# Kernel optimization log

Hardware: AMD Instinct MI355X
Metric: run time of the kernel (lower is better)

## Reference

```python
import jax, jax.numpy as jnp
import numpy as np

B, H, W, NC = 8, 64, 64, 128
INTER = NC // 2
BN_EPS = 1e-4


def setup_inputs() -> dict:
    key = jax.random.key(0)
    ks = jax.random.split(key, 6)
    s_in = 1.0 / np.sqrt(NC)
    s_w = 1.0 / np.sqrt(INTER)
    return {
        "x": jax.random.normal(ks[0], (B, H, W, NC), jnp.float32),
        "theta_w": jax.random.normal(ks[1], (NC, INTER), jnp.float32) * s_in,
        "theta_b": jnp.zeros((INTER,), jnp.float32),
        "phi_w": jax.random.normal(ks[2], (NC, INTER), jnp.float32) * s_in,
        "phi_b": jnp.zeros((INTER,), jnp.float32),
        "g_w": jax.random.normal(ks[3], (NC, INTER), jnp.float32) * s_in,
        "g_b": jnp.zeros((INTER,), jnp.float32),
        "W_w": jax.random.normal(ks[4], (INTER, NC), jnp.float32) * s_w,
        "W_b": jnp.zeros((NC,), jnp.float32),
        "bn_gamma": jnp.ones((NC,), jnp.float32),
        "bn_beta": jnp.zeros((NC,), jnp.float32),
        "bn_mean": jnp.zeros((NC,), jnp.float32),
        "bn_var": jax.random.uniform(ks[5], (NC,), jnp.float32, 0.5, 1.5),
    }


def reference(x, theta_w, theta_b, phi_w, phi_b, g_w, g_b, W_w, W_b,
              bn_gamma, bn_beta, bn_mean, bn_var):
    b, h, w, c = x.shape
    n = h * w
    # 1x1 conv projections == per-pixel GEMMs; flatten spatial to tokens
    xt = x.reshape(b, n, c)                                  # [B, N, C]
    theta = xt @ theta_w + theta_b                           # [B, N, C']
    phi = xt @ phi_w + phi_b                                 # [B, N, C']
    g = xt @ g_w + g_b                                       # [B, N, C']
    # single-head, unscaled non-local attention
    f = jnp.einsum("bnc,bmc->bnm", theta, phi)               # [B, N, N]
    attn = jax.nn.softmax(f, axis=-1)
    y = jnp.einsum("bnm,bmc->bnc", attn, g)                  # [B, N, C']
    # W: 1x1 conv back to nc + BatchNorm (inference), then residual
    wy = y @ W_w + W_b                                       # [B, N, C]
    inv = bn_gamma * jax.lax.rsqrt(bn_var + BN_EPS)
    wy = (wy - bn_mean) * inv + bn_beta
    z = wy.reshape(b, h, w, c) + x
    return z
```

## Files before the change

### kernel.cpp

```cpp
#include <hip/hip_runtime.h>
#include <math.h>

typedef _Float16 v8h __attribute__((ext_vector_type(8)));
typedef __fp16 h2 __attribute__((ext_vector_type(2)));
typedef float v4f __attribute__((ext_vector_type(4)));
typedef float v16f __attribute__((ext_vector_type(16)));

#define MFMA32(a, b, c) __builtin_amdgcn_mfma_f32_32x32x16_f16((a), (b), (c), 0, 0, 0)
#define MFMA16(a, b, c) __builtin_amdgcn_mfma_f32_16x16x32_f16((a), (b), (c), 0, 0, 0)
#define ZV4 ((v4f){0.f, 0.f, 0.f, 0.f})
#define LOG2E 1.44269504f

#define TA64(row, colb)  ((((row) * 128) + (colb)) ^ (((row) & 7) << 4))
#define TA128(row, colb) ((((row) * 256) + (colb)) ^ (((row) & 15) << 4))

#define RAW_BARRIER() do {                                        \
    asm volatile("s_waitcnt lgkmcnt(0)" ::: "memory");            \
    asm volatile("s_barrier" ::: "memory");                       \
} while (0)

__device__ __forceinline__ unsigned int pk_f16(float a, float b) {
    return __builtin_bit_cast(unsigned int, __builtin_amdgcn_cvt_pkrtz(a, b));
}
__device__ __forceinline__ void pl32swap(unsigned int& a, unsigned int& b) {
    asm("v_permlane32_swap_b32 %0, %1" : "+v"(a), "+v"(b));
}
__device__ __forceinline__ float fexp2(float x) {
    float r;
    asm("v_exp_f32 %0, %1" : "=v"(r) : "v"(x));
    return r;
}

__global__ __launch_bounds__(256) void k_prep(
    const float* __restrict__ tw, const float* __restrict__ pw,
    const float* __restrict__ gw,
    const float* __restrict__ Ww, const float* __restrict__ Wb,
    const float* __restrict__ gamma, const float* __restrict__ beta,
    const float* __restrict__ mean, const float* __restrict__ var,
    _Float16* __restrict__ Wt, _Float16* __restrict__ wallT,
    float* __restrict__ sc, float* __restrict__ bi)
{
    int gid = blockIdx.x * 256 + threadIdx.x;
    #pragma unroll
    for (int r = 0; r < 2; ++r) {
        int idx = r * 4096 + gid;
        int d = idx >> 7, c = idx & 127;
        Wt[c * 64 + d] = (_Float16)Ww[idx];
    }
    #pragma unroll
    for (int r = 0; r < 6; ++r) {
        int idx = r * 4096 + gid;
        int p = idx >> 13, rem = idx & 8191;
        int o = rem >> 7, k = rem & 127;
        const float* wm = (p == 0) ? tw : (p == 1) ? pw : gw;
        wallT[idx] = (_Float16)wm[k * 64 + o];
    }
    if (blockIdx.x == 0 && threadIdx.x < 128) {
        int c = threadIdx.x;
        float inv = gamma[c] * rsqrtf(var[c] + 1e-4f);
        sc[c] = inv;
        bi[c] = (Wb[c] - mean[c]) * inv + beta[c];
    }
}

__global__ __launch_bounds__(512, 4) void k_proj(
    const float* __restrict__ x, const _Float16* __restrict__ wallT,
    const float* __restrict__ tb, const float* __restrict__ pb,
    const float* __restrict__ gb,
    _Float16* __restrict__ theta, _Float16* __restrict__ phi,
    _Float16* __restrict__ gT)
{
    __shared__ __align__(16) _Float16 tsc[8][16 * 72];
    __shared__ __align__(16) _Float16 gblk[64][136];
    const int t = threadIdx.x;
    const int w = t >> 6, l = t & 63, h = l >> 4, lo = l & 15;
    const int tok0 = blockIdx.x * 128 + w * 16;
    _Float16* tw_l = &tsc[w][0];

    v8h xA[4];
    #pragma unroll
    for (int kc = 0; kc < 4; ++kc) {
        const float* px = x + (size_t)(tok0 + lo) * 128 + kc * 32 + h * 8;
        float4 f0 = *(const float4*)(px);
        float4 f1 = *(const float4*)(px + 4);
        uint4 u;
        u.x = pk_f16(f0.x, f0.y); u.y = pk_f16(f0.z, f0.w);
        u.z = pk_f16(f1.x, f1.y); u.w = pk_f16(f1.z, f1.w);
        xA[kc] = __builtin_bit_cast(v8h, u);
    }

    #pragma unroll
    for (int p = 0; p < 2; ++p) {
        const _Float16* wp = wallT + p * 8192;
        const float* bias = (p == 0) ? tb : pb;
        _Float16* dst = (p == 0) ? theta : phi;
        const float scale = (p == 0) ? LOG2E : 1.0f;
        #pragma unroll
        for (int oc = 0; oc < 4; ++oc) {
            int o = oc * 16 + lo;
            v4f acc = ZV4;
            #pragma unroll
            for (int kc = 0; kc < 4; ++kc) {
                v8h B = *(const v8h*)(wp + o * 128 + kc * 32 + h * 8);
                acc = MFMA16(xA[kc], B, acc);
            }
            float bv = bias[o];
            #pragma unroll
            for (int rr = 0; rr < 4; ++rr)
                tw_l[(4 * h + rr) * 72 + o] = (_Float16)((acc[rr] + bv) * scale);
        }
        int token = l >> 2, c = l & 3;
        v8h v0 = *(const v8h*)&tw_l[token * 72 + c * 16];
        v8h v1 = *(const v8h*)&tw_l[token * 72 + c * 16 + 8];
        _Float16* dp = dst + (size_t)(tok0 + token) * 64 + c * 16;
        *(v8h*)(dp) = v0;
        *(v8h*)(dp + 8) = v1;
    }
    {
        const _Float16* wp = wallT + 2 * 8192;
        #pragma unroll
        for (int oc = 0; oc < 4; ++oc) {
            v4f acc = ZV4;
            #pragma unroll
            for (int kc = 0; kc < 4; ++kc) {
                v8h A = *(const v8h*)(wp + (oc * 16 + lo) * 128 + kc * 32 + h * 8);
                acc = MFMA16(A, xA[kc], acc);
            }
            #pragma unroll
            for (int rr = 0; rr < 4; ++rr) {
                int o = oc * 16 + 4 * h + rr;
                gblk[o][w * 16 + lo] = (_Float16)(acc[rr] + gb[o]);
            }
        }
    }
    __syncthreads();
    {
        int o = t >> 3, ch = t & 7;
        v8h v0 = *(const v8h*)&gblk[o][ch * 16];
        v8h v1 = *(const v8h*)&gblk[o][ch * 16 + 8];
        int tokg0 = blockIdx.x * 128;
        int bb = tokg0 >> 12, n0 = (tokg0 & 4095) + ch * 16;
        _Float16* gp = gT + ((size_t)bb * 64 + o) * 4096 + n0;
        *(v8h*)(gp) = v0;
        *(v8h*)(gp + 8) = v1;
    }
}

__global__ __launch_bounds__(512, 2) void k_attn(
    const _Float16* __restrict__ theta,
    const _Float16* __restrict__ phi,
    const _Float16* __restrict__ gT,
    const _Float16* __restrict__ Wt,
    const float* __restrict__ sc, const float* __restrict__ bi,
    const float* __restrict__ x, float* __restrict__ out)
{
    __shared__ __align__(16) _Float16 ldsbuf[32768];
    __shared__ float zf[8 * 64];

    const int t = threadIdx.x;
    const int w = t >> 6, l = t & 63, q32 = l & 31, hi2 = l >> 5;
    const int qp = w & 1, kh = w >> 1;
    const int bid = blockIdx.x;
    const int b = bid & 7, qb = bid >> 3;
    const size_t tok0 = (size_t)b * 4096 + qb * 128;

    char* phB = (char*)ldsbuf;
    char* gvB = (char*)ldsbuf + 32768;

    v8h thB[2][4];
    #pragma unroll
    for (int f = 0; f < 2; ++f)
        #pragma unroll
        for (int kc = 0; kc < 4; ++kc)
            thB[f][kc] = *(const v8h*)(theta +
                (tok0 + qp * 64 + f * 32 + q32) * 64 + kc * 16 + hi2 * 8);

    const _Float16* phb = phi + (size_t)b * 4096 * 64;
    const _Float16* gvb = gT + (size_t)b * 64 * 4096;

    v16f yacc[2][2];
    #pragma unroll
    for (int f = 0; f < 2; ++f)
        #pragma unroll
        for (int df = 0; df < 2; ++df)
            #pragma unroll
            for (int r = 0; r < 16; ++r) yacc[f][df][r] = 0.f;
    float mrow[2] = {-INFINITY, -INFINITY}, lpart[2] = {0.f, 0.f};

    int qkRd[4], gvRd[2][2];
    #pragma unroll
    for (int kc = 0; kc < 4; ++kc)
        qkRd[kc] = TA64(kh * 32 + q32, (kc * 16 + hi2 * 8) * 2);
    #pragma unroll
    for (int df = 0; df < 2; ++df)
        #pragma unroll
        for (int s = 0; s < 2; ++s)
            gvRd[df][s] = TA128(df * 32 + q32, (kh * 32 + s * 16 + hi2 * 8) * 2);

    const int phA0 = TA64(t >> 3, (t & 7) * 16);
    const int phA1 = TA64((t >> 3) + 64, (t & 7) * 16);
    const int gvA0 = TA128(t >> 4, (t & 15) * 16);
    const int gvA1 = TA128((t >> 4) + 32, (t & 15) * 16);
    const _Float16* pPh = phb + (size_t)(t >> 3) * 64 + (t & 7) * 8;
    const _Float16* pGv = gvb + (size_t)(t >> 4) * 4096 + (t & 15) * 8;

    v8h pf0 = *(const v8h*)(pPh);
    v8h pf1 = *(const v8h*)(pPh + 64 * 64);
    v8h pf2 = *(const v8h*)(pGv);
    v8h pf3 = *(const v8h*)(pGv + (size_t)32 * 4096);
    pPh += 8192; pGv += 128;

    for (int kt = 0; kt < 32; ++kt) {
        char* phL = phB + (kt & 1) * 16384;
        char* gvL = gvB + (kt & 1) * 16384;
        *(v8h*)(phL + phA0) = pf0;
        *(v8h*)(phL + phA1) = pf1;
        *(v8h*)(gvL + gvA0) = pf2;
        *(v8h*)(gvL + gvA1) = pf3;
        if (kt < 31) {
            pf0 = *(const v8h*)(pPh);
            pf1 = *(const v8h*)(pPh + 64 * 64);
            pf2 = *(const v8h*)(pGv);
            pf3 = *(const v8h*)(pGv + (size_t)32 * 4096);
            pPh += 8192; pGv += 128;
        }
        RAW_BARRIER();
        v16f S0, S1;
        #pragma unroll
        for (int r = 0; r < 16; ++r) { S0[r] = 0.f; S1[r] = 0.f; }
        __builtin_amdgcn_s_setprio(1);
        #pragma unroll
        for (int kc = 0; kc < 4; ++kc) {
            v8h A = *(const v8h*)(phL + qkRd[kc]);
            S0 = MFMA32(A, thB[0][kc], S0);
            S1 = MFMA32(A, thB[1][kc], S1);
        }
        __builtin_amdgcn_s_setprio(0);
        v8h gA[2][2];
        #pragma unroll
        for (int df = 0; df < 2; ++df)
            #pragma unroll
            for (int s = 0; s < 2; ++s)
                gA[df][s] = *(const v8h*)(gvL + gvRd[df][s]);
        float vmax[2];
        {
            float a0 = fmaxf(fmaxf(S0[0], S0[1]), S0[2]);
            float a1 = fmaxf(fmaxf(S0[3], S0[4]), S0[5]);
            float a2 = fmaxf(fmaxf(S0[6], S0[7]), S0[8]);
            float a3 = fmaxf(fmaxf(S0[9], S0[10]), S0[11]);
            float a4 = fmaxf(fmaxf(S0[12], S0[13]), S0[14]);
            float v = fmaxf(fmaxf(fmaxf(a0, a1), fmaxf(a2, a3)),
                            fmaxf(a4, S0[15]));
            vmax[0] = fmaxf(v, __shfl_xor(v, 32));
        }
        {
            float a0 = fmaxf(fmaxf(S1[0], S1[1]), S1[2]);
            float a1 = fmaxf(fmaxf(S1[3], S1[4]), S1[5]);
            float a2 = fmaxf(fmaxf(S1[6], S1[7]), S1[8]);
            float a3 = fmaxf(fmaxf(S1[9], S1[10]), S1[11]);
            float a4 = fmaxf(fmaxf(S1[12], S1[13]), S1[14]);
            float v = fmaxf(fmaxf(fmaxf(a0, a1), fmaxf(a2, a3)),
                            fmaxf(a4, S1[15]));
            vmax[1] = fmaxf(v, __shfl_xor(v, 32));
        }
        bool ok = (vmax[0] <= mrow[0] + 11.54f) && (vmax[1] <= mrow[1] + 11.54f);
        if (!__all(ok)) {
            #pragma unroll
            for (int f = 0; f < 2; ++f) {
                float mn = fmaxf(mrow[f], vmax[f]);
                float aa = fexp2(mrow[f] - mn);
                mrow[f] = mn;
                lpart[f] *= aa;
                #pragma unroll
                for (int df = 0; df < 2; ++df)
                    #pragma unroll
                    for (int r = 0; r < 16; ++r)
                        yacc[f][df][r] *= aa;
            }
        }
        const h2 one2 = {(__fp16)1.0f, (__fp16)1.0f};
        {
            #pragma unroll
            for (int r = 0; r < 16; ++r) S0[r] = fexp2(S0[r] - mrow[0]);
            float psum = 0.f;
            h2 pk[8];
            #pragma unroll
            for (int j = 0; j < 8; ++j) {
                pk[j] = __builtin_amdgcn_cvt_pkrtz(S0[2 * j], S0[2 * j + 1]);
                psum = __builtin_amdgcn_fdot2(pk[j], one2, psum, false);
            }
            lpart[0] += psum;
            unsigned int W0 = __builtin_bit_cast(unsigned int, pk[0]);
            unsigned int W1 = __builtin_bit_cast(unsigned int, pk[1]);
            unsigned int W2 = __builtin_bit_cast(unsigned int, pk[2]);
            unsigned int W3 = __builtin_bit_cast(unsigned int, pk[3]);
            unsigned int W4 = __builtin_bit_cast(unsigned int, pk[4]);
            unsigned int W5 = __builtin_bit_cast(unsigned int, pk[5]);
            unsigned int W6 = __builtin_bit_cast(unsigned int, pk[6]);
            unsigned int W7 = __builtin_bit_cast(unsigned int, pk[7]);
            pl32swap(W0, W2); pl32swap(W1, W3);
            pl32swap(W4, W6); pl32swap(W5, W7);
            uint4 u1; u1.x = W0; u1.y = W1; u1.z = W2; u1.w = W3;
            uint4 u2; u2.x = W4; u2.y = W5; u2.z = W6; u2.w = W7;
            v8h pB0 = __builtin_bit_cast(v8h, u1);
            v8h pB1 = __builtin_bit_cast(v8h, u2);
            __builtin_amdgcn_s_setprio(1);
            yacc[0][0] = MFMA32(gA[0][0], pB0, yacc[0][0]);
            yacc[0][0] = MFMA32(gA[0][1], pB1, yacc[0][0]);
            yacc[0][1] = MFMA32(gA[1][0], pB0, yacc[0][1]);
            yacc[0][1] = MFMA32(gA[1][1], pB1, yacc[0][1]);
            __builtin_amdgcn_s_setprio(0);
        }
        {
            #pragma unroll
            for (int r = 0; r < 16; ++r) S1[r] = fexp2(S1[r] - mrow[1]);
            float psum = 0.f;
            h2 pk[8];
            #pragma unroll
            for (int j = 0; j < 8; ++j) {
                pk[j] = __builtin_amdgcn_cvt_pkrtz(S1[2 * j], S1[2 * j + 1]);
                psum = __builtin_amdgcn_fdot2(pk[j], one2, psum, false);
            }
            lpart[1] += psum;
            unsigned int W0 = __builtin_bit_cast(unsigned int, pk[0]);
            unsigned int W1 = __builtin_bit_cast(unsigned int, pk[1]);
            unsigned int W2 = __builtin_bit_cast(unsigned int, pk[2]);
            unsigned int W3 = __builtin_bit_cast(unsigned int, pk[3]);
            unsigned int W4 = __builtin_bit_cast(unsigned int, pk[4]);
            unsigned int W5 = __builtin_bit_cast(unsigned int, pk[5]);
            unsigned int W6 = __builtin_bit_cast(unsigned int, pk[6]);
            unsigned int W7 = __builtin_bit_cast(unsigned int, pk[7]);
            pl32swap(W0, W2); pl32swap(W1, W3);
            pl32swap(W4, W6); pl32swap(W5, W7);
            uint4 u1; u1.x = W0; u1.y = W1; u1.z = W2; u1.w = W3;
            uint4 u2; u2.x = W4; u2.y = W5; u2.z = W6; u2.w = W7;
            v8h pB0 = __builtin_bit_cast(v8h, u1);
            v8h pB1 = __builtin_bit_cast(v8h, u2);
            __builtin_amdgcn_s_setprio(1);
            yacc[1][0] = MFMA32(gA[0][0], pB0, yacc[1][0]);
            yacc[1][0] = MFMA32(gA[0][1], pB1, yacc[1][0]);
            yacc[1][1] = MFMA32(gA[1][0], pB0, yacc[1][1]);
            yacc[1][1] = MFMA32(gA[1][1], pB1, yacc[1][1]);
            __builtin_amdgcn_s_setprio(0);
        }
    }

    __syncthreads();
    #pragma unroll
    for (int f = 0; f < 2; ++f) {
        float lrow = lpart[f] + __shfl_xor(lpart[f], 32);
        float inv = 1.0f / lrow;
        char* slot = (char*)ldsbuf + w * 8192 + f * 4096 + l * 64;
        #pragma unroll
        for (int j = 0; j < 4; ++j) {
            int df = j >> 1, r0 = (j & 1) * 8;
            uint4 u;
            u.x = pk_f16(yacc[f][df][r0 + 0] * inv, yacc[f][df][r0 + 1] * inv);
            u.y = pk_f16(yacc[f][df][r0 + 2] * inv, yacc[f][df][r0 + 3] * inv);
            u.z = pk_f16(yacc[f][df][r0 + 4] * inv, yacc[f][df][r0 + 5] * inv);
            u.w = pk_f16(yacc[f][df][r0 + 6] * inv, yacc[f][df][r0 + 7] * inv);
            *(uint4*)(slot + (j * 16 ^ ((l & 3) << 4))) = u;
        }
        zf[(w * 2 + f) * 32 + q32] = mrow[f] + __log2f(lrow);
    }
    __syncthreads();
    if (w >= 2) return;

    #pragma unroll
    for (int f = 0; f < 2; ++f) {
        float zq[4];
        #pragma unroll
        for (int kp = 0; kp < 4; ++kp)
            zq[kp] = zf[((kp * 2 + w) * 2 + f) * 32 + q32];
        float zmx = fmaxf(fmaxf(zq[0], zq[1]), fmaxf(zq[2], zq[3]));
        float wsum = 0.f;
        float yfin[2][16];
        #pragma unroll
        for (int df = 0; df < 2; ++df)
            #pragma unroll
            for (int r = 0; r < 16; ++r) yfin[df][r] = 0.f;
        #pragma unroll
        for (int kp = 0; kp < 4; ++kp) {
            char* slot = (char*)ldsbuf + (kp * 2 + w) * 8192 + f * 4096 + l * 64;
            float wk = fexp2(zq[kp] - zmx);
            wsum += wk;
            #pragma unroll
            for (int j = 0; j < 4; ++j) {
                v8h c = *(const v8h*)(slot + (j * 16 ^ ((l & 3) << 4)));
                int df = j >> 1, r0 = (j & 1) * 8;
                #pragma unroll
                for (int e = 0; e < 8; ++e)
                    yfin[df][r0 + e] += wk * (float)c[e];
            }
        }
        float nrm = 1.0f / wsum;
        v8h yA[4];
        #pragma unroll
        for (int kc = 0; kc < 4; ++kc) {
            int df = kc >> 1, r0 = (kc & 1) * 8;
            unsigned int Wa = pk_f16(yfin[df][r0 + 0] * nrm, yfin[df][r0 + 1] * nrm);
            unsigned int Wb2 = pk_f16(yfin[df][r0 + 2] * nrm, yfin[df][r0 + 3] * nrm);
            unsigned int Wc = pk_f16(yfin[df][r0 + 4] * nrm, yfin[df][r0 + 5] * nrm);
            unsigned int Wd = pk_f16(yfin[df][r0 + 6] * nrm, yfin[df][r0 + 7] * nrm);
            pl32swap(Wa, Wc); pl32swap(Wb2, Wd);
            uint4 u; u.x = Wa; u.y = Wb2; u.z = Wc; u.w = Wd;
            yA[kc] = __builtin_bit_cast(v8h, u);
        }
        const int tokA = qb * 128 + w * 64 + f * 32;
        const float* xb = x + (size_t)b * 4096 * 128;
        float* ob = out + (size_t)b * 4096 * 128;
        #pragma unroll
        for (int cf = 0; cf < 4; ++cf) {
            int c = cf * 32 + q32;
            v16f wy;
            #pragma unroll
            for (int r = 0; r < 16; ++r) wy[r] = 0.f;
            #pragma unroll
            for (int kc = 0; kc < 4; ++kc) {
                v8h wB = *(const v8h*)(Wt + c * 64 + kc * 16 + hi2 * 8);
                wy = MFMA32(yA[kc], wB, wy);
            }
            float scc = sc[c], bic = bi[c];
            #pragma unroll
            for (int r = 0; r < 16; ++r) {
                int qrow = (r & 3) + 8 * (r >> 2) + 4 * hi2;
                size_t off = (size_t)(tokA + qrow) * 128 + c;
                ob[off] = wy[r] * scc + bic + xb[off];
            }
        }
    }
}

extern "C" void kernel_launch(void* const* d_in, const int* in_sizes, int n_in,
                              void* d_out, int out_size, void* d_ws, size_t ws_size,
                              hipStream_t stream) {
    const float* x     = (const float*)d_in[0];
    const float* tw    = (const float*)d_in[1];
    const float* tb    = (const float*)d_in[2];
    const float* pw    = (const float*)d_in[3];
    const float* pb    = (const float*)d_in[4];
    const float* gw    = (const float*)d_in[5];
    const float* gb    = (const float*)d_in[6];
    const float* Ww    = (const float*)d_in[7];
    const float* Wb    = (const float*)d_in[8];
    const float* gamma = (const float*)d_in[9];
    const float* beta  = (const float*)d_in[10];
    const float* mean  = (const float*)d_in[11];
    const float* var   = (const float*)d_in[12];

    char* ws = (char*)d_ws;
    _Float16* theta = (_Float16*)ws;
    _Float16* phi   = (_Float16*)(ws + (4u << 20));
    _Float16* gT    = (_Float16*)(ws + (8u << 20));
    _Float16* Wt    = (_Float16*)(ws + (12u << 20));
    _Float16* wallT = (_Float16*)(ws + (12u << 20) + (1u << 16));
    float* sc       = (float*)(ws + (12u << 20) + (2u << 16));
    float* bi       = sc + 128;

    k_prep<<<16, 256, 0, stream>>>(tw, pw, gw, Ww, Wb, gamma, beta, mean, var,
                                   Wt, wallT, sc, bi);
    k_proj<<<256, 512, 0, stream>>>(x, wallT, tb, pb, gb, theta, phi, gT);
    k_attn<<<256, 512, 0, stream>>>(theta, phi, gT, Wt, sc, bi,
                                    x, (float*)d_out);
}
```

Measured before the change: 82.28 us.

## Halve attention block to 64 queries with single-buffered LDS tiles

The attention kernel now uses 256-thread blocks that each handle 64 query tokens, launched as 512 blocks instead of 256 blocks of 512 threads. Each wave owns a 32-key slice of every 128-key tile. The double-buffered phi/g LDS staging becomes a single buffer: the next tile is loaded into registers after the compute and written to LDS between two barriers. The goal is to spread work over more blocks and cut LDS per block, at the cost of losing load/compute overlap, adding a barrier per iteration and re-reading each key tile from L2 twice as often.

```diff
diff --git a/kernel.cpp b/kernel.cpp
--- a/kernel.cpp
+++ b/kernel.cpp
@@ -146,7 +146,7 @@
     }
 }
 
-__global__ __launch_bounds__(512, 2) void k_attn(
+__global__ __launch_bounds__(256, 4) void k_attn(
     const _Float16* __restrict__ theta,
     const _Float16* __restrict__ phi,
     const _Float16* __restrict__ gT,
@@ -154,18 +154,18 @@
     const float* __restrict__ sc, const float* __restrict__ bi,
     const float* __restrict__ x, float* __restrict__ out)
 {
-    __shared__ __align__(16) _Float16 ldsbuf[32768];
-    __shared__ float zf[8 * 64];
+    __shared__ __align__(16) _Float16 ldsbuf[16384];
+    __shared__ float zf[4 * 64];
 
     const int t = threadIdx.x;
     const int w = t >> 6, l = t & 63, q32 = l & 31, hi2 = l >> 5;
-    const int qp = w & 1, kh = w >> 1;
+    const int kh = w;
     const int bid = blockIdx.x;
     const int b = bid & 7, qb = bid >> 3;
-    const size_t tok0 = (size_t)b * 4096 + qb * 128;
-
-    char* phB = (char*)ldsbuf;
-    char* gvB = (char*)ldsbuf + 32768;
+    const size_t tok0 = (size_t)b * 4096 + qb * 64;
+
+    char* phC = (char*)ldsbuf;
+    char* gvC = (char*)ldsbuf + 16384;
 
     v8h thB[2][4];
     #pragma unroll
@@ -173,7 +173,7 @@
         #pragma unroll
         for (int kc = 0; kc < 4; ++kc)
             thB[f][kc] = *(const v8h*)(theta +
-                (tok0 + qp * 64 + f * 32 + q32) * 64 + kc * 16 + hi2 * 8);
+                (tok0 + f * 32 + q32) * 64 + kc * 16 + hi2 * 8);
 
     const _Float16* phb = phi + (size_t)b * 4096 * 64;
     const _Float16* gvb = gT + (size_t)b * 64 * 4096;
@@ -197,41 +197,32 @@
         for (int s = 0; s < 2; ++s)
             gvRd[df][s] = TA128(df * 32 + q32, (kh * 32 + s * 16 + hi2 * 8) * 2);
 
-    const int phA0 = TA64(t >> 3, (t & 7) * 16);
-    const int phA1 = TA64((t >> 3) + 64, (t & 7) * 16);
-    const int gvA0 = TA128(t >> 4, (t & 15) * 16);
-    const int gvA1 = TA128((t >> 4) + 32, (t & 15) * 16);
+    int phA[4], gvA[4];
+    #pragma unroll
+    for (int j = 0; j < 4; ++j) {
+        phA[j] = TA64(j * 32 + (t >> 3), (t & 7) * 16);
+        gvA[j] = TA128(j * 16 + (t >> 4), (t & 15) * 16);
+    }
     const _Float16* pPh = phb + (size_t)(t >> 3) * 64 + (t & 7) * 8;
     const _Float16* pGv = gvb + (size_t)(t >> 4) * 4096 + (t & 15) * 8;
 
-    v8h pf0 = *(const v8h*)(pPh);
-    v8h pf1 = *(const v8h*)(pPh + 64 * 64);
-    v8h pf2 = *(const v8h*)(pGv);
-    v8h pf3 = *(const v8h*)(pGv + (size_t)32 * 4096);
-    pPh += 8192; pGv += 128;
+    {
+        #pragma unroll
+        for (int j = 0; j < 4; ++j) {
+            *(v8h*)(phC + phA[j]) = *(const v8h*)(pPh + j * 2048);
+            *(v8h*)(gvC + gvA[j]) = *(const v8h*)(pGv + (size_t)j * 65536);
+        }
+    }
+    RAW_BARRIER();
 
     for (int kt = 0; kt < 32; ++kt) {
-        char* phL = phB + (kt & 1) * 16384;
-        char* gvL = gvB + (kt & 1) * 16384;
-        *(v8h*)(phL + phA0) = pf0;
-        *(v8h*)(phL + phA1) = pf1;
-        *(v8h*)(gvL + gvA0) = pf2;
-        *(v8h*)(gvL + gvA1) = pf3;
-        if (kt < 31) {
-            pf0 = *(const v8h*)(pPh);
-            pf1 = *(const v8h*)(pPh + 64 * 64);
-            pf2 = *(const v8h*)(pGv);
-            pf3 = *(const v8h*)(pGv + (size_t)32 * 4096);
-            pPh += 8192; pGv += 128;
-        }
-        RAW_BARRIER();
         v16f S0, S1;
         #pragma unroll
         for (int r = 0; r < 16; ++r) { S0[r] = 0.f; S1[r] = 0.f; }
         __builtin_amdgcn_s_setprio(1);
         #pragma unroll
         for (int kc = 0; kc < 4; ++kc) {
-            v8h A = *(const v8h*)(phL + qkRd[kc]);
+            v8h A = *(const v8h*)(phC + qkRd[kc]);
             S0 = MFMA32(A, thB[0][kc], S0);
             S1 = MFMA32(A, thB[1][kc], S1);
         }
@@ -241,7 +232,7 @@
         for (int df = 0; df < 2; ++df)
             #pragma unroll
             for (int s = 0; s < 2; ++s)
-                gA[df][s] = *(const v8h*)(gvL + gvRd[df][s]);
+                gA[df][s] = *(const v8h*)(gvC + gvRd[df][s]);
         float vmax[2];
         {
             float a0 = fmaxf(fmaxf(S0[0], S0[1]), S0[2]);
@@ -343,9 +334,33 @@
             yacc[1][1] = MFMA32(gA[1][1], pB1, yacc[1][1]);
             __builtin_amdgcn_s_setprio(0);
         }
-    }
-
-    __syncthreads();
+        v8h np0, np1, np2, np3, ng0, ng1, ng2, ng3;
+        if (kt < 31) {
+            const _Float16* pp = pPh + (size_t)(kt + 1) * 8192;
+            np0 = *(const v8h*)(pp);
+            np1 = *(const v8h*)(pp + 2048);
+            np2 = *(const v8h*)(pp + 4096);
+            np3 = *(const v8h*)(pp + 6144);
+            const _Float16* pg = pGv + (size_t)(kt + 1) * 128;
+            ng0 = *(const v8h*)(pg);
+            ng1 = *(const v8h*)(pg + 65536);
+            ng2 = *(const v8h*)(pg + 131072);
+            ng3 = *(const v8h*)(pg + 196608);
+        }
+        RAW_BARRIER();
+        if (kt < 31) {
+            *(v8h*)(phC + phA[0]) = np0;
+            *(v8h*)(phC + phA[1]) = np1;
+            *(v8h*)(phC + phA[2]) = np2;
+            *(v8h*)(phC + phA[3]) = np3;
+            *(v8h*)(gvC + gvA[0]) = ng0;
+            *(v8h*)(gvC + gvA[1]) = ng1;
+            *(v8h*)(gvC + gvA[2]) = ng2;
+            *(v8h*)(gvC + gvA[3]) = ng3;
+        }
+        RAW_BARRIER();
+    }
+
     #pragma unroll
     for (int f = 0; f < 2; ++f) {
         float lrow = lpart[f] + __shfl_xor(lpart[f], 32);
@@ -366,12 +381,12 @@
     __syncthreads();
     if (w >= 2) return;
 
-    #pragma unroll
-    for (int f = 0; f < 2; ++f) {
+    {
+        const int f = w;
         float zq[4];
         #pragma unroll
         for (int kp = 0; kp < 4; ++kp)
-            zq[kp] = zf[((kp * 2 + w) * 2 + f) * 32 + q32];
+            zq[kp] = zf[(kp * 2 + f) * 32 + q32];
         float zmx = fmaxf(fmaxf(zq[0], zq[1]), fmaxf(zq[2], zq[3]));
         float wsum = 0.f;
         float yfin[2][16];
@@ -381,7 +396,7 @@
             for (int r = 0; r < 16; ++r) yfin[df][r] = 0.f;
         #pragma unroll
         for (int kp = 0; kp < 4; ++kp) {
-            char* slot = (char*)ldsbuf + (kp * 2 + w) * 8192 + f * 4096 + l * 64;
+            char* slot = (char*)ldsbuf + kp * 8192 + f * 4096 + l * 64;
             float wk = fexp2(zq[kp] - zmx);
             wsum += wk;
             #pragma unroll
@@ -406,7 +421,7 @@
             uint4 u; u.x = Wa; u.y = Wb2; u.z = Wc; u.w = Wd;
             yA[kc] = __builtin_bit_cast(v8h, u);
         }
-        const int tokA = qb * 128 + w * 64 + f * 32;
+        const int tokA = qb * 64 + f * 32;
         const float* xb = x + (size_t)b * 4096 * 128;
         float* ob = out + (size_t)b * 4096 * 128;
         #pragma unroll
@@ -460,6 +475,6 @@
     k_prep<<<16, 256, 0, stream>>>(tw, pw, gw, Ww, Wb, gamma, beta, mean, var,
                                    Wt, wallT, sc, bi);
     k_proj<<<256, 512, 0, stream>>>(x, wallT, tb, pb, gb, theta, phi, gT);
-    k_attn<<<256, 512, 0, stream>>>(theta, phi, gT, Wt, sc, bi,
+    k_attn<<<512, 256, 0, stream>>>(theta, phi, gT, Wt, sc, bi,
                                     x, (float*)d_out);
 }
```

After: 216.5 us. 2.63x slower.
